# Performance work log

Hardware: AMD Instinct MI355X
Metric: run time of the kernel (lower is better)

## Reference

```python
import jax, jax.numpy as jnp
import numpy as np

DIM, R, HEAD = 512, 4, 8
HD = DIM // HEAD
SCALE = HD ** -0.5
EPS = 1e-5


def dwconv(x, w, b, stride, padding):
    # depthwise conv (groups == channels) + bias + relu; x:[B,C,H,W], w:[C,1,kh,kw]
    y = jax.lax.conv_general_dilated(
        x, w, window_strides=stride, padding=padding,
        feature_group_count=x.shape[1],
        dimension_numbers=('NCHW', 'OIHW', 'NCHW'))
    return jax.nn.relu(y + b[None, :, None, None])


def setup_inputs() -> dict:
    key = jax.random.key(0)
    ks = jax.random.split(key, 12)
    s = 0.02
    return {
        'x': jax.random.normal(ks[0], (8, DIM, 56, 56), dtype=jnp.float32),
        'Wq': jax.random.normal(ks[1], (DIM, DIM), dtype=jnp.float32) * s,
        'bq': jnp.zeros((DIM,), jnp.float32),
        'Wkv': jax.random.normal(ks[2], (2 * DIM, DIM), dtype=jnp.float32) * s,
        'bkv': jnp.zeros((2 * DIM,), jnp.float32),
        'w1a': jax.random.normal(ks[3], (DIM, 1, 1, R), dtype=jnp.float32) * s,
        'b1a': jnp.zeros((DIM,), jnp.float32),
        'w1b': jax.random.normal(ks[4], (DIM, 1, R, 1), dtype=jnp.float32) * s,
        'b1b': jnp.zeros((DIM,), jnp.float32),
        'w2': jax.random.normal(ks[5], (DIM, 1, R, R), dtype=jnp.float32) * s,
        'b2': jnp.zeros((DIM,), jnp.float32),
        'w3': jax.random.normal(ks[6], (DIM, 1, 3, 3), dtype=jnp.float32) * s,
        'b3': jnp.zeros((DIM,), jnp.float32),
        'gamma': jnp.ones((DIM,), jnp.float32),
        'beta': jnp.zeros((DIM,), jnp.float32),
    }


def reference(x, Wq, bq, Wkv, bkv, w1a, b1a, w1b, b1b, w2, b2, w3, b3, gamma, beta):
    B, C, H, W = x.shape
    N = H * W
    x_layer = x.reshape(B, C, N).transpose(0, 2, 1)  # [B,N,C]
    q = (x_layer @ Wq.T + bq).reshape(B, N, HEAD, HD).transpose(0, 2, 1, 3)  # [B,h,N,d]

    # branch 1: (1,R)s(1,R) dwconv -> (R,1)s(R,1) dwconv
    l1 = dwconv(dwconv(x, w1a, b1a, (1, R), ((0, 0), (0, 0))),
                w1b, b1b, (R, 1), ((0, 0), (0, 0))).reshape(B, C, -1)
    # branch 2: RxR stride-R dwconv
    l2 = dwconv(x, w2, b2, (R, R), ((0, 0), (0, 0))).reshape(B, C, -1)
    # branch 3: avg-pool to (H/R, W/R) then 3x3 dwconv pad 1
    l3 = x.reshape(B, C, H // R, R, W // R, R).mean(axis=(3, 5))
    l3 = dwconv(l3, w3, b3, (1, 1), ((1, 1), (1, 1))).reshape(B, C, -1)

    l_ = jnp.concatenate([l1, l2, l3], axis=2).transpose(0, 2, 1)  # [B,M,C]
    mu = l_.mean(-1, keepdims=True)
    var = ((l_ - mu) ** 2).mean(-1, keepdims=True)
    l_ = (l_ - mu) * jax.lax.rsqrt(var + EPS) * gamma + beta

    M = l_.shape[1]
    kv = (l_ @ Wkv.T + bkv).reshape(B, M, 2, HEAD, HD).transpose(2, 0, 3, 1, 4)
    k, v = kv[0], kv[1]  # [B,h,M,d]

    attn = jax.nn.softmax(jnp.einsum('bhid,bhjd->bhij', q, k) * SCALE, axis=-1)
    out = jnp.einsum('bhij,bhjd->bhid', attn, v).transpose(0, 2, 1, 3).reshape(B, N, C)
    # NOTE: original torch code computes proj(out) but then overwrites it with
    # proj_drop(out); with drop=0 the returned value is exactly `out`.
    return out
```

## Files before the change

kernel.cpp:

```cpp
#include <hip/hip_runtime.h>
#include <hip/hip_bf16.h>

#define BATCH   8
#define C_DIM   512
#define HWD     56
#define NPIX    3136
#define PW      14
#define PP      196
#define M_TOT   588
#define BM_ROWS 4704
#define BM_PAD  4736
#define HEADS   8
#define HD      64
#define N_SEQ   3136
#define SM_SCALE 0.125f
#define SM_SCALE_LOG2E 0.1803368801111204f

#define KS_STRIDE 68
#define KS_ROWS   592
#define VS_STRIDE 596
#define ATTN_LDS_SHORTS (KS_ROWS * KS_STRIDE + 64 * VS_STRIDE)
#define ATTN_LDS_BYTES  (ATTN_LDS_SHORTS * 2)

typedef __attribute__((ext_vector_type(8))) short bf16x8;
typedef __attribute__((ext_vector_type(4))) short bf16x4;
typedef __attribute__((ext_vector_type(4))) float f32x4;

__device__ __forceinline__ short f2bs(float f) {
    __hip_bfloat16 h = __float2bfloat16(f);
    return *reinterpret_cast<short*>(&h);
}
__device__ __forceinline__ unsigned pkbf(float lo, float hi) {
    __hip_bfloat162 t = __float22bfloat162_rn(make_float2(lo, hi));
    return *reinterpret_cast<unsigned*>(&t);
}
__device__ __forceinline__ float fexp2(float x) {
#if __has_builtin(__builtin_amdgcn_exp2f)
    return __builtin_amdgcn_exp2f(x);
#else
    return exp2f(x);
#endif
}

__device__ __forceinline__ f32x4 mfma16(bf16x4 a, bf16x4 b, f32x4 c) {
#if __has_builtin(__builtin_amdgcn_mfma_f32_16x16x16bf16_1k)
    return __builtin_amdgcn_mfma_f32_16x16x16bf16_1k(a, b, c, 0, 0, 0);
#elif __has_builtin(__builtin_amdgcn_mfma_f32_16x16x16_bf16)
    return __builtin_amdgcn_mfma_f32_16x16x16_bf16(a, b, c, 0, 0, 0);
#else
    asm volatile("v_mfma_f32_16x16x16_bf16 %0, %1, %2, %0\n\ts_nop 7\n\ts_nop 1"
                 : "+v"(c) : "v"(a), "v"(b));
    return c;
#endif
}

__device__ __forceinline__ void gl_lds16(const void* g, void* l) {
    __builtin_amdgcn_global_load_lds(
        (const __attribute__((address_space(1))) void*)g,
        (__attribute__((address_space(3))) void*)l, 16, 0, 0);
}


__device__ __forceinline__ void branches_body(
    int c, int b, int tid, float* sbuf,
    const float* __restrict__ x,
    const float* __restrict__ w1a, const float* __restrict__ b1a,
    const float* __restrict__ w1b, const float* __restrict__ b1b,
    const float* __restrict__ w2,  const float* __restrict__ b2,
    const float* __restrict__ w3,  const float* __restrict__ b3,
    float* __restrict__ l_pre)
{
    float* xs    = sbuf;
    float* y1s   = sbuf + 3136;
    float* pools = sbuf + 3920;
    const float* xp = x + ((size_t)(b * C_DIM + c)) * NPIX;
    for (int i = tid; i < NPIX / 4; i += 256)
        ((float4*)xs)[i] = ((const float4*)xp)[i];
    __syncthreads();

    const float wa0 = w1a[c*4+0], wa1 = w1a[c*4+1], wa2 = w1a[c*4+2], wa3 = w1a[c*4+3];
    const float ba = b1a[c];
    for (int i = tid; i < HWD * PW; i += 256) {
        int h = i / PW, w = i % PW;
        const float* r = xs + h * HWD + w * 4;
        float v = ba + r[0]*wa0 + r[1]*wa1 + r[2]*wa2 + r[3]*wa3;
        y1s[i] = fmaxf(v, 0.f);
    }
    if (tid < PP) {
        int h = tid / PW, w = tid % PW;
        float s = 0.f;
        #pragma unroll
        for (int r = 0; r < 4; ++r) {
            const float* rr = xs + (h*4 + r) * HWD + w * 4;
            s += rr[0] + rr[1] + rr[2] + rr[3];
        }
        pools[tid] = s * (1.f / 16.f);
    }
    __syncthreads();

    if (tid < PP) {
        int h = tid / PW, w = tid % PW;
        float* lp = l_pre + ((size_t)(b * C_DIM + c)) * M_TOT;
        float v1 = b1b[c];
        v1 += y1s[(h*4+0)*PW + w] * w1b[c*4+0];
        v1 += y1s[(h*4+1)*PW + w] * w1b[c*4+1];
        v1 += y1s[(h*4+2)*PW + w] * w1b[c*4+2];
        v1 += y1s[(h*4+3)*PW + w] * w1b[c*4+3];
        lp[tid] = fmaxf(v1, 0.f);
        float v2 = b2[c];
        #pragma unroll
        for (int r = 0; r < 4; ++r)
            #pragma unroll
            for (int s2 = 0; s2 < 4; ++s2)
                v2 += xs[(h*4+r)*HWD + w*4 + s2] * w2[c*16 + r*4 + s2];
        lp[PP + tid] = fmaxf(v2, 0.f);
        float v3 = b3[c];
        #pragma unroll
        for (int dh = -1; dh <= 1; ++dh)
            #pragma unroll
            for (int dw = -1; dw <= 1; ++dw) {
                int hh = h + dh, ww = w + dw;
                if (hh >= 0 && hh < PW && ww >= 0 && ww < PW)
                    v3 += pools[hh*PW + ww] * w3[c*9 + (dh+1)*3 + (dw+1)];
            }
        lp[2*PP + tid] = fmaxf(v3, 0.f);
    }
}

__device__ __forceinline__ void xpose_body(
    int bx, int by, int bz, int tid, float* sbuf,
    const float* __restrict__ x, short* __restrict__ Xb)
{
    float (*sx)[68] = (float(*)[68])sbuf;
    const int n0 = bx * 64, c0 = by * 64, b = bz;
    #pragma unroll
    for (int it = 0; it < 4; ++it) {
        int idx = tid + it * 256;
        int cr = idx >> 4, n4 = (idx & 15) * 4;
        float4 v = *(const float4*)(x + ((size_t)(b * C_DIM + c0 + cr)) * NPIX + n0 + n4);
        *(float4*)&sx[cr][n4] = v;
    }
    __syncthreads();
    #pragma unroll
    for (int p = 0; p < 2; ++p) {
        int idx = tid + p * 256;
        int nr = idx >> 3, cg = (idx & 7) * 8;
        short ov[8];
        #pragma unroll
        for (int e = 0; e < 8; ++e) ov[e] = f2bs(sx[cg + e][nr]);
        *(float4*)&Xb[((size_t)(b * NPIX + n0 + nr)) * C_DIM + c0 + cg] = *(float4*)ov;
    }
}

__device__ __forceinline__ void wconv_body(
    int blk, int tid,
    const float* __restrict__ Wq, const float* __restrict__ Wkv,
    short* __restrict__ Wqb, short* __restrict__ Wkvb)
{
    int i = (blk * 256 + tid) * 4;
    if (i < 262144) {
        float4 v = *(const float4*)(Wq + i);
        short o[4] = {f2bs(v.x), f2bs(v.y), f2bs(v.z), f2bs(v.w)};
        *(short4*)(Wqb + i) = *(short4*)o;
    } else {
        int j = i - 262144;
        float4 v = *(const float4*)(Wkv + j);
        short o[4] = {f2bs(v.x), f2bs(v.y), f2bs(v.z), f2bs(v.w)};
        *(short4*)(Wkvb + j) = *(short4*)o;
    }
}

__global__ __launch_bounds__(256) void k_front(
    const float* __restrict__ x,
    const float* __restrict__ Wq, const float* __restrict__ Wkv,
    short* __restrict__ Wqb, short* __restrict__ Wkvb,
    short* __restrict__ Xb,
    const float* __restrict__ w1a, const float* __restrict__ b1a,
    const float* __restrict__ w1b, const float* __restrict__ b1b,
    const float* __restrict__ w2,  const float* __restrict__ b2,
    const float* __restrict__ w3,  const float* __restrict__ b3,
    float* __restrict__ l_pre)
{
    __shared__ float sbuf[4368];
    const int bid = blockIdx.x, tid = threadIdx.x;
    if (bid < 4096) {
        branches_body(bid & 511, bid >> 9, tid, sbuf,
                      x, w1a, b1a, w1b, b1b, w2, b2, w3, b3, l_pre);
    } else if (bid < 7232) {
        int i2 = bid - 4096;
        xpose_body(i2 % 49, (i2 / 49) & 7, i2 / 392, tid, sbuf, x, Xb);
    } else {
        wconv_body(bid - 7232, tid, Wq, Wkv, Wqb, Wkvb);
    }
}


__device__ __forceinline__ void gemm_q_body(
    int bx, int by, int tid, short* As, short* Bs,
    const short* __restrict__ A, const short* __restrict__ Bw,
    const float* __restrict__ bias, short* __restrict__ Qb)
{
    const int lane = tid & 63, w = tid >> 6;
    const int l15 = lane & 15, quad = lane >> 4;
    const int wr = w & 1, wc = w >> 1;
    const int row0 = bx * 128, col0 = by * 128;
    const int lr8 = lane >> 3, lc8 = (lane & 7) * 8;

    f32x4 acc[4][4] = {};

    for (int c0 = 0; c0 < 512; c0 += 64) {
        __syncthreads();
        #pragma unroll
        for (int it = 0; it < 4; ++it) {
            int r = w * 32 + it * 8;
            gl_lds16(A  + (size_t)(row0 + r + lr8) * 512 + c0 + lc8, &As[r * 64]);
            gl_lds16(Bw + (size_t)(col0 + r + lr8) * 512 + c0 + lc8, &Bs[r * 64]);
        }
        __syncthreads();
        #pragma unroll
        for (int ks = 0; ks < 2; ++ks) {
            bf16x8 af[4], bf[4];
            #pragma unroll
            for (int t = 0; t < 4; ++t) {
                af[t] = *(const bf16x8*)&As[(wr*64 + t*16 + l15)*64 + ks*32 + quad*8];
                bf[t] = *(const bf16x8*)&Bs[(wc*64 + t*16 + l15)*64 + ks*32 + quad*8];
            }
            #pragma unroll
            for (int nt = 0; nt < 4; ++nt)
                #pragma unroll
                for (int mt = 0; mt < 4; ++mt)
                    acc[nt][mt] = __builtin_amdgcn_mfma_f32_16x16x32_bf16(
                        af[nt], bf[mt], acc[nt][mt], 0, 0, 0);
        }
    }

    #pragma unroll
    for (int nt = 0; nt < 4; ++nt) {
        int row_t = row0 + wr * 64 + nt * 16 + quad * 4;
        #pragma unroll
        for (int mt = 0; mt < 4; ++mt) {
            int col = col0 + wc * 64 + mt * 16 + l15;
            float bv = bias[col];
            int h = col >> 6, d = col & 63;
            #pragma unroll
            for (int r = 0; r < 4; ++r) {
                int row_g = row_t + r;
                int b = row_g / N_SEQ;
                int n = row_g - b * N_SEQ;
                Qb[(((size_t)(b * HEADS + h)) * N_SEQ + n) * HD + d] =
                    f2bs((acc[nt][mt][r] + bv) * SM_SCALE_LOG2E);
            }
        }
    }
}

__device__ __forceinline__ void stats_body(
    int sx_, int sb_, int tid, float* red,
    const float* __restrict__ l_pre, float2* __restrict__ stats)
{
    float* ssum = red;
    float* ssq  = red + 256;
    const int ml = tid & 63, cg = tid >> 6;
    const int b = sb_;
    const int m = sx_ * 64 + ml;
    float s = 0.f, q = 0.f;
    if (m < M_TOT) {
        const float* base = l_pre + ((size_t)b * C_DIM + cg * 128) * M_TOT + m;
        for (int c = 0; c < 128; ++c) {
            float v = base[(size_t)c * M_TOT];
            s += v; q += v * v;
        }
    }
    ssum[cg*64 + ml] = s; ssq[cg*64 + ml] = q;
    __syncthreads();
    if (tid < 64 && sx_ * 64 + tid < M_TOT) {
        float ts = ssum[tid] + ssum[64+tid] + ssum[128+tid] + ssum[192+tid];
        float tq = ssq[tid] + ssq[64+tid] + ssq[128+tid] + ssq[192+tid];
        float mu = ts * (1.f / 512.f);
        float var = tq * (1.f / 512.f) - mu * mu;
        stats[(size_t)b * M_TOT + sx_ * 64 + tid] =
            make_float2(mu, rsqrtf(var + 1e-5f));
    }
}

__global__ __launch_bounds__(256) void k_mid(
    const short* __restrict__ Xb, const short* __restrict__ Wqb,
    const float* __restrict__ bq, short* __restrict__ Qb,
    const float* __restrict__ l_pre, float2* __restrict__ stats)
{
    __shared__ short sb2[16384];
    const int bid = blockIdx.x, tid = threadIdx.x;
    if (bid < 784) {
        gemm_q_body(bid % 196, bid / 196, tid, sb2, sb2 + 8192,
                    Xb, Wqb, bq, Qb);
    } else {
        int sid = bid - 784;
        stats_body(sid % 10, sid / 10, tid, (float*)sb2, l_pre, stats);
    }
}

__global__ __launch_bounds__(256) void k_lnt(
    const float* __restrict__ l_pre, const float2* __restrict__ stats,
    const float* __restrict__ gamma, const float* __restrict__ beta,
    short* __restrict__ Lb)
{
    __shared__ float sx[64][68];
    const int tid = threadIdx.x;
    const int m0 = blockIdx.x * 64, c0 = blockIdx.y * 64, b = blockIdx.z;
    #pragma unroll
    for (int it = 0; it < 4; ++it) {
        int idx = tid + it * 256;
        int cr = idx >> 4, m4 = (idx & 15) * 4;
        float4 v = {0.f, 0.f, 0.f, 0.f};
        if (m0 + m4 < M_TOT)
            v = *(const float4*)(l_pre + ((size_t)(b * C_DIM + c0 + cr)) * M_TOT + m0 + m4);
        *(float4*)&sx[cr][m4] = v;
    }
    __syncthreads();
    #pragma unroll
    for (int p = 0; p < 2; ++p) {
        int idx = tid + p * 256;
        int mr = idx >> 3, cg = (idx & 7) * 8;
        int m = m0 + mr;
        float mu = 0.f, rstd = 0.f;
        if (m < M_TOT) {
            float2 st = stats[(size_t)b * M_TOT + m];
            mu = st.x; rstd = st.y;
        }
        short ov[8];
        #pragma unroll
        for (int e = 0; e < 8; ++e) {
            int c = c0 + cg + e;
            ov[e] = f2bs((sx[cg + e][mr] - mu) * rstd * gamma[c] + beta[c]);
        }
        if (m < M_TOT)
            *(float4*)&Lb[((size_t)(b * M_TOT + m)) * C_DIM + c0 + cg] = *(float4*)ov;
    }
}

__global__ __launch_bounds__(256) void k_gemm_kv(
    const short* __restrict__ A, const short* __restrict__ Bw,
    const float* __restrict__ bias,
    short* __restrict__ Kb, short* __restrict__ Vt)
{
    __shared__ short As[128 * 64];
    __shared__ short Bs[128 * 64];
    const int tid = threadIdx.x;
    const int lane = tid & 63, w = tid >> 6;
    const int l15 = lane & 15, quad = lane >> 4;
    const int wr = w & 1, wc = w >> 1;
    const int row0 = blockIdx.x * 128, col0 = blockIdx.y * 128;
    const int lr8 = lane >> 3, lc8 = (lane & 7) * 8;

    f32x4 acc[4][4] = {};

    for (int c0 = 0; c0 < 512; c0 += 64) {
        __syncthreads();
        #pragma unroll
        for (int it = 0; it < 4; ++it) {
            int r = w * 32 + it * 8;
            gl_lds16(A  + (size_t)(row0 + r + lr8) * 512 + c0 + lc8, &As[r * 64]);
            gl_lds16(Bw + (size_t)(col0 + r + lr8) * 512 + c0 + lc8, &Bs[r * 64]);
        }
        __syncthreads();
        #pragma unroll
        for (int ks = 0; ks < 2; ++ks) {
            bf16x8 af[4], bf[4];
            #pragma unroll
            for (int t = 0; t < 4; ++t) {
                af[t] = *(const bf16x8*)&As[(wr*64 + t*16 + l15)*64 + ks*32 + quad*8];
                bf[t] = *(const bf16x8*)&Bs[(wc*64 + t*16 + l15)*64 + ks*32 + quad*8];
            }
            #pragma unroll
            for (int nt = 0; nt < 4; ++nt)
                #pragma unroll
                for (int mt = 0; mt < 4; ++mt)
                    acc[nt][mt] = __builtin_amdgcn_mfma_f32_16x16x32_bf16(
                        af[nt], bf[mt], acc[nt][mt], 0, 0, 0);
        }
    }

    #pragma unroll
    for (int nt = 0; nt < 4; ++nt) {
        int row_t = row0 + wr * 64 + nt * 16 + quad * 4;
        #pragma unroll
        for (int mt = 0; mt < 4; ++mt) {
            int col = col0 + wc * 64 + mt * 16 + l15;
            float bv = bias[col];
            #pragma unroll
            for (int r = 0; r < 4; ++r) {
                int row_g = row_t + r;
                float v = acc[nt][mt][r] + bv;
                if (row_g < BM_ROWS) {
                    int b = row_g / M_TOT;
                    int m = row_g - b * M_TOT;
                    if (col < 512) {
                        int h = col >> 6, d = col & 63;
                        Kb[(((size_t)(b * HEADS + h)) * M_TOT + m) * HD + d] = f2bs(v);
                    } else {
                        int jj = col - 512, h = jj >> 6, d = jj & 63;
                        Vt[(((size_t)(b * HEADS + h)) * HD + d) * M_TOT + m] = f2bs(v);
                    }
                }
            }
        }
    }
}

__global__ __launch_bounds__(1024) void k_attn(
    const short* __restrict__ Qb, const short* __restrict__ Kb,
    const short* __restrict__ Vt, float* __restrict__ out)
{
    extern __shared__ short smem[];
    short* Ks = smem;
    short* Vs = smem + KS_ROWS * KS_STRIDE;

    const int tid = threadIdx.x;
    const int lane = tid & 63, w = tid >> 6;
    const int l15 = lane & 15, quad = lane >> 4;
    const int q4 = blockIdx.x, h = blockIdx.y, b = blockIdx.z;
    const size_t bh = (size_t)(b * HEADS + h);
    const size_t kbase = bh * M_TOT * HD;
    const size_t vbase = bh * (size_t)HD * M_TOT;

    for (int i = tid; i < 4704; i += 1024) {
        int row = i >> 3, seg = i & 7;
        *(float4*)&Ks[row * KS_STRIDE + seg * 8] =
            *(const float4*)(Kb + kbase + (size_t)row * 64 + seg * 8);
    }
    if (tid < 256) {
        int r = tid >> 6, cc = tid & 63;
        Ks[(588 + r) * KS_STRIDE + cc] = 0;
    }
    {
        int row = tid >> 4, tg = tid & 15;
        const short* src = Vt + vbase + (size_t)row * M_TOT;
        #pragma unroll 2
        for (int jj = tg; jj < 147; jj += 16)
            *(float2*)&Vs[row * VS_STRIDE + jj * 4] = *(const float2*)(src + jj * 4);
    }
    if (tid < 512) {
        int row = tid >> 3, cc = tid & 7;
        Vs[row * VS_STRIDE + 588 + cc] = 0;
    }
    __syncthreads();

    const bf16x4 ones = {(short)0x3F80, (short)0x3F80, (short)0x3F80, (short)0x3F80};

    for (int ds = w; ds < 25; ds += 16) {
        const bool sbv = (ds < 24);
        const int nA = q4 * 784 + ds * 32 + l15;
        const int nB = sbv ? nA + 16 : nA;

        bf16x8 qfA[2], qfB[2];
        #pragma unroll
        for (int ks = 0; ks < 2; ++ks) {
            qfA[ks] = *(const bf16x8*)(Qb + (bh * N_SEQ + nA) * HD + ks * 32 + quad * 8);
            qfB[ks] = *(const bf16x8*)(Qb + (bh * N_SEQ + nB) * HD + ks * 32 + quad * 8);
        }

        f32x4 oaccA[4] = {}, oaccB[4] = {};
        f32x4 rsaccA = {}, rsaccB = {};

        auto LOAD = [&](int j0, bf16x8& K0, bf16x8& K1,
                        bf16x4& V0, bf16x4& V1, bf16x4& V2, bf16x4& V3) {
            const short* kr = &Ks[(j0 + l15) * KS_STRIDE + quad * 8];
            K0 = *(const bf16x8*)kr;
            K1 = *(const bf16x8*)(kr + 32);
            const short* vr = &Vs[l15 * VS_STRIDE + j0 + quad * 4];
            V0 = *(const bf16x4*)vr;
            V1 = *(const bf16x4*)(vr + 16 * VS_STRIDE);
            V2 = *(const bf16x4*)(vr + 32 * VS_STRIDE);
            V3 = *(const bf16x4*)(vr + 48 * VS_STRIDE);
        };

        auto STEP = [&](bf16x8 K0, bf16x8 K1,
                        bf16x4 V0, bf16x4 V1, bf16x4 V2, bf16x4 V3) {
            f32x4 sA = {}, sB = {};
            __builtin_amdgcn_s_setprio(1);
            sA = __builtin_amdgcn_mfma_f32_16x16x32_bf16(K0, qfA[0], sA, 0, 0, 0);
            sB = __builtin_amdgcn_mfma_f32_16x16x32_bf16(K0, qfB[0], sB, 0, 0, 0);
            sA = __builtin_amdgcn_mfma_f32_16x16x32_bf16(K1, qfA[1], sA, 0, 0, 0);
            sB = __builtin_amdgcn_mfma_f32_16x16x32_bf16(K1, qfB[1], sB, 0, 0, 0);
            __builtin_amdgcn_s_setprio(0);

            float pA[4], pB[4];
            #pragma unroll
            for (int r = 0; r < 4; ++r) {
                pA[r] = fexp2(sA[r]);
                pB[r] = fexp2(sB[r]);
            }
            unsigned ua[2] = {pkbf(pA[0], pA[1]), pkbf(pA[2], pA[3])};
            unsigned ub[2] = {pkbf(pB[0], pB[1]), pkbf(pB[2], pB[3])};
            bf16x4 pbA, pbB;
            __builtin_memcpy(&pbA, ua, 8);
            __builtin_memcpy(&pbB, ub, 8);

            __builtin_amdgcn_s_setprio(1);
            rsaccA = mfma16(ones, pbA, rsaccA);
            rsaccB = mfma16(ones, pbB, rsaccB);

            oaccA[0] = mfma16(V0, pbA, oaccA[0]);
            oaccB[0] = mfma16(V0, pbB, oaccB[0]);
            oaccA[1] = mfma16(V1, pbA, oaccA[1]);
            oaccB[1] = mfma16(V1, pbB, oaccB[1]);
            oaccA[2] = mfma16(V2, pbA, oaccA[2]);
            oaccB[2] = mfma16(V2, pbB, oaccB[2]);
            oaccA[3] = mfma16(V3, pbA, oaccA[3]);
            oaccB[3] = mfma16(V3, pbB, oaccB[3]);
            __builtin_amdgcn_s_setprio(0);
        };

        bf16x8 k0a, k1a, k0b, k1b;
        bf16x4 v0a, v1a, v2a, v3a, v0b, v1b, v2b, v3b;

        LOAD(0, k0a, k1a, v0a, v1a, v2a, v3a);
        __builtin_amdgcn_sched_barrier(0);
        #pragma unroll 1
        for (int t = 0; t < 18; ++t) {
            const int j0 = t * 32;
            LOAD(j0 + 16, k0b, k1b, v0b, v1b, v2b, v3b);
            __builtin_amdgcn_sched_barrier(0);
            STEP(k0a, k1a, v0a, v1a, v2a, v3a);
            LOAD(j0 + 32, k0a, k1a, v0a, v1a, v2a, v3a);
            __builtin_amdgcn_sched_barrier(0);
            STEP(k0b, k1b, v0b, v1b, v2b, v3b);
        }
        STEP(k0a, k1a, v0a, v1a, v2a, v3a);

        const float invA = 1.f / (rsaccA[0] - 4.f);
        const float invB = 1.f / (rsaccB[0] - 4.f);
        float* orowA = out + ((size_t)b * N_SEQ + nA) * C_DIM + h * HD;
        #pragma unroll
        for (int dt = 0; dt < 4; ++dt) {
            float4 o;
            o.x = oaccA[dt][0] * invA; o.y = oaccA[dt][1] * invA;
            o.z = oaccA[dt][2] * invA; o.w = oaccA[dt][3] * invA;
            *(float4*)&orowA[dt * 16 + quad * 4] = o;
        }
        if (sbv) {
            float* orowB = out + ((size_t)b * N_SEQ + nB) * C_DIM + h * HD;
            #pragma unroll
            for (int dt = 0; dt < 4; ++dt) {
                float4 o;
                o.x = oaccB[dt][0] * invB; o.y = oaccB[dt][1] * invB;
                o.z = oaccB[dt][2] * invB; o.w = oaccB[dt][3] * invB;
                *(float4*)&orowB[dt * 16 + quad * 4] = o;
            }
        }
    }
}

extern "C" void kernel_launch(void* const* d_in, const int* in_sizes, int n_in,
                              void* d_out, int out_size, void* d_ws, size_t ws_size,
                              hipStream_t stream) {
    const float* x     = (const float*)d_in[0];
    const float* Wq    = (const float*)d_in[1];
    const float* bq    = (const float*)d_in[2];
    const float* Wkv   = (const float*)d_in[3];
    const float* bkv   = (const float*)d_in[4];
    const float* w1a   = (const float*)d_in[5];
    const float* b1a   = (const float*)d_in[6];
    const float* w1b   = (const float*)d_in[7];
    const float* b1b   = (const float*)d_in[8];
    const float* w2    = (const float*)d_in[9];
    const float* b2    = (const float*)d_in[10];
    const float* w3    = (const float*)d_in[11];
    const float* b3    = (const float*)d_in[12];
    const float* gamma = (const float*)d_in[13];
    const float* beta  = (const float*)d_in[14];
    float* out = (float*)d_out;

    char* ws = (char*)d_ws;
    short*  Xb    = (short*)ws;
    short*  Wqb   = (short*)(ws + 25690112);
    short*  Wkvb  = (short*)(ws + 26214400);
    float*  l_pre = (float*)(ws + 27262976);
    short*  Kb    = (short*)(ws + 27262976);
    short*  Vt    = (short*)(ws + 32079872);
    short*  Qb    = (short*)(ws + 36896768);
    float2* stats = (float2*)d_out;
    short*  Lb    = (short*)((char*)d_out + 65536);

    hipFuncSetAttribute((const void*)k_attn,
                        hipFuncAttributeMaxDynamicSharedMemorySize,
                        ATTN_LDS_BYTES);

    k_front<<<8000, 256, 0, stream>>>(
        x, Wq, Wkv, Wqb, Wkvb, Xb,
        w1a, b1a, w1b, b1b, w2, b2, w3, b3, l_pre);
    k_mid<<<864, 256, 0, stream>>>(Xb, Wqb, bq, Qb, l_pre, stats);
    k_lnt<<<dim3(10, 8, BATCH), 256, 0, stream>>>(l_pre, stats, gamma, beta, Lb);
    k_gemm_kv<<<dim3(37, 8), 256, 0, stream>>>(Lb, Wkvb, bkv, Kb, Vt);
    k_attn<<<dim3(4, HEADS, BATCH), 1024, ATTN_LDS_BYTES, stream>>>(Qb, Kb, Vt, out);
}
```

Before: 257.3 us.

## Load GEMM operands directly from global, swizzle block order, drop attention setprio

The Q and KV GEMMs stop staging tiles through LDS with global_load_lds and barriers. Each lane now reads its MFMA fragments straight from global memory, relying on L1/L2 for reuse. Block indices are remapped into groups of 8 row tiles that share column tiles, to improve L2 locality, with padding blocks that exit early. The s_setprio hints around the MFMA groups in the attention kernel are removed. The risks are more global traffic, uncoalesced 16-byte loads per lane, and a changed wave scheduling balance in attention.

After: 311.6 us. 21.1% more time.

```diff
diff --git a/kernel.cpp b/kernel.cpp
--- a/kernel.cpp
+++ b/kernel.cpp
@@ -54,12 +54,6 @@
 #endif
 }
 
-__device__ __forceinline__ void gl_lds16(const void* g, void* l) {
-    __builtin_amdgcn_global_load_lds(
-        (const __attribute__((address_space(1))) void*)g,
-        (__attribute__((address_space(3))) void*)l, 16, 0, 0);
-}
-
 
 __device__ __forceinline__ void branches_body(
     int c, int b, int tid, float* sbuf,
@@ -196,7 +190,7 @@
 
 
 __device__ __forceinline__ void gemm_q_body(
-    int bx, int by, int tid, short* As, short* Bs,
+    int bx, int by, int tid,
     const short* __restrict__ A, const short* __restrict__ Bw,
     const float* __restrict__ bias, short* __restrict__ Qb)
 {
@@ -204,34 +198,30 @@
     const int l15 = lane & 15, quad = lane >> 4;
     const int wr = w & 1, wc = w >> 1;
     const int row0 = bx * 128, col0 = by * 128;
-    const int lr8 = lane >> 3, lc8 = (lane & 7) * 8;
+
+    const short* arow[4];
+    const short* brow[4];
+    #pragma unroll
+    for (int t = 0; t < 4; ++t) {
+        arow[t] = A  + (size_t)(row0 + wr*64 + t*16 + l15) * 512 + quad * 8;
+        brow[t] = Bw + (size_t)(col0 + wc*64 + t*16 + l15) * 512 + quad * 8;
+    }
 
     f32x4 acc[4][4] = {};
-
-    for (int c0 = 0; c0 < 512; c0 += 64) {
-        __syncthreads();
-        #pragma unroll
-        for (int it = 0; it < 4; ++it) {
-            int r = w * 32 + it * 8;
-            gl_lds16(A  + (size_t)(row0 + r + lr8) * 512 + c0 + lc8, &As[r * 64]);
-            gl_lds16(Bw + (size_t)(col0 + r + lr8) * 512 + c0 + lc8, &Bs[r * 64]);
-        }
-        __syncthreads();
-        #pragma unroll
-        for (int ks = 0; ks < 2; ++ks) {
-            bf16x8 af[4], bf[4];
-            #pragma unroll
-            for (int t = 0; t < 4; ++t) {
-                af[t] = *(const bf16x8*)&As[(wr*64 + t*16 + l15)*64 + ks*32 + quad*8];
-                bf[t] = *(const bf16x8*)&Bs[(wc*64 + t*16 + l15)*64 + ks*32 + quad*8];
-            }
-            #pragma unroll
-            for (int nt = 0; nt < 4; ++nt)
-                #pragma unroll
-                for (int mt = 0; mt < 4; ++mt)
-                    acc[nt][mt] = __builtin_amdgcn_mfma_f32_16x16x32_bf16(
-                        af[nt], bf[mt], acc[nt][mt], 0, 0, 0);
-        }
+    #pragma unroll 4
+    for (int kk = 0; kk < 16; ++kk) {
+        bf16x8 af[4], bf[4];
+        #pragma unroll
+        for (int t = 0; t < 4; ++t) {
+            af[t] = *(const bf16x8*)(arow[t] + kk * 32);
+            bf[t] = *(const bf16x8*)(brow[t] + kk * 32);
+        }
+        #pragma unroll
+        for (int nt = 0; nt < 4; ++nt)
+            #pragma unroll
+            for (int mt = 0; mt < 4; ++mt)
+                acc[nt][mt] = __builtin_amdgcn_mfma_f32_16x16x32_bf16(
+                    af[nt], bf[mt], acc[nt][mt], 0, 0, 0);
     }
 
     #pragma unroll
@@ -288,14 +278,16 @@
     const float* __restrict__ bq, short* __restrict__ Qb,
     const float* __restrict__ l_pre, float2* __restrict__ stats)
 {
-    __shared__ short sb2[16384];
+    __shared__ float sred[512];
     const int bid = blockIdx.x, tid = threadIdx.x;
-    if (bid < 784) {
-        gemm_q_body(bid % 196, bid / 196, tid, sb2, sb2 + 8192,
-                    Xb, Wqb, bq, Qb);
+    if (bid < 800) {
+        int bx = (bid >> 5) * 8 + (bid & 7);
+        int by = (bid >> 3) & 3;
+        if (bx < 196)
+            gemm_q_body(bx, by, tid, Xb, Wqb, bq, Qb);
     } else {
-        int sid = bid - 784;
-        stats_body(sid % 10, sid / 10, tid, (float*)sb2, l_pre, stats);
+        int sid = bid - 800;
+        stats_body(sid % 10, sid / 10, tid, sred, l_pre, stats);
     }
 }
 
@@ -343,41 +335,39 @@
     const float* __restrict__ bias,
     short* __restrict__ Kb, short* __restrict__ Vt)
 {
-    __shared__ short As[128 * 64];
-    __shared__ short Bs[128 * 64];
-    const int tid = threadIdx.x;
+    const int bid = blockIdx.x, tid = threadIdx.x;
+    const int bx = (bid >> 6) * 8 + (bid & 7);
+    const int by = (bid >> 3) & 7;
+    if (bx >= 37) return;
+
     const int lane = tid & 63, w = tid >> 6;
     const int l15 = lane & 15, quad = lane >> 4;
     const int wr = w & 1, wc = w >> 1;
-    const int row0 = blockIdx.x * 128, col0 = blockIdx.y * 128;
-    const int lr8 = lane >> 3, lc8 = (lane & 7) * 8;
+    const int row0 = bx * 128, col0 = by * 128;
+
+    const short* arow[4];
+    const short* brow[4];
+    #pragma unroll
+    for (int t = 0; t < 4; ++t) {
+        arow[t] = A  + (size_t)(row0 + wr*64 + t*16 + l15) * 512 + quad * 8;
+        brow[t] = Bw + (size_t)(col0 + wc*64 + t*16 + l15) * 512 + quad * 8;
+    }
 
     f32x4 acc[4][4] = {};
-
-    for (int c0 = 0; c0 < 512; c0 += 64) {
-        __syncthreads();
-        #pragma unroll
-        for (int it = 0; it < 4; ++it) {
-            int r = w * 32 + it * 8;
-            gl_lds16(A  + (size_t)(row0 + r + lr8) * 512 + c0 + lc8, &As[r * 64]);
-            gl_lds16(Bw + (size_t)(col0 + r + lr8) * 512 + c0 + lc8, &Bs[r * 64]);
-        }
-        __syncthreads();
-        #pragma unroll
-        for (int ks = 0; ks < 2; ++ks) {
-            bf16x8 af[4], bf[4];
-            #pragma unroll
-            for (int t = 0; t < 4; ++t) {
-                af[t] = *(const bf16x8*)&As[(wr*64 + t*16 + l15)*64 + ks*32 + quad*8];
-                bf[t] = *(const bf16x8*)&Bs[(wc*64 + t*16 + l15)*64 + ks*32 + quad*8];
-            }
-            #pragma unroll
-            for (int nt = 0; nt < 4; ++nt)
-                #pragma unroll
-                for (int mt = 0; mt < 4; ++mt)
-                    acc[nt][mt] = __builtin_amdgcn_mfma_f32_16x16x32_bf16(
-                        af[nt], bf[mt], acc[nt][mt], 0, 0, 0);
-        }
+    #pragma unroll 4
+    for (int kk = 0; kk < 16; ++kk) {
+        bf16x8 af[4], bf[4];
+        #pragma unroll
+        for (int t = 0; t < 4; ++t) {
+            af[t] = *(const bf16x8*)(arow[t] + kk * 32);
+            bf[t] = *(const bf16x8*)(brow[t] + kk * 32);
+        }
+        #pragma unroll
+        for (int nt = 0; nt < 4; ++nt)
+            #pragma unroll
+            for (int mt = 0; mt < 4; ++mt)
+                acc[nt][mt] = __builtin_amdgcn_mfma_f32_16x16x32_bf16(
+                    af[nt], bf[mt], acc[nt][mt], 0, 0, 0);
     }
 
     #pragma unroll
@@ -477,12 +467,10 @@
         auto STEP = [&](bf16x8 K0, bf16x8 K1,
                         bf16x4 V0, bf16x4 V1, bf16x4 V2, bf16x4 V3) {
             f32x4 sA = {}, sB = {};
-            __builtin_amdgcn_s_setprio(1);
             sA = __builtin_amdgcn_mfma_f32_16x16x32_bf16(K0, qfA[0], sA, 0, 0, 0);
             sB = __builtin_amdgcn_mfma_f32_16x16x32_bf16(K0, qfB[0], sB, 0, 0, 0);
             sA = __builtin_amdgcn_mfma_f32_16x16x32_bf16(K1, qfA[1], sA, 0, 0, 0);
             sB = __builtin_amdgcn_mfma_f32_16x16x32_bf16(K1, qfB[1], sB, 0, 0, 0);
-            __builtin_amdgcn_s_setprio(0);
 
             float pA[4], pB[4];
             #pragma unroll
@@ -496,7 +484,6 @@
             __builtin_memcpy(&pbA, ua, 8);
             __builtin_memcpy(&pbB, ub, 8);
 
-            __builtin_amdgcn_s_setprio(1);
             rsaccA = mfma16(ones, pbA, rsaccA);
             rsaccB = mfma16(ones, pbB, rsaccB);
 
@@ -508,7 +495,6 @@
             oaccB[2] = mfma16(V2, pbB, oaccB[2]);
             oaccA[3] = mfma16(V3, pbA, oaccA[3]);
             oaccB[3] = mfma16(V3, pbB, oaccB[3]);
-            __builtin_amdgcn_s_setprio(0);
         };
 
         bf16x8 k0a, k1a, k0b, k1b;
@@ -589,8 +575,8 @@
     k_front<<<8000, 256, 0, stream>>>(
         x, Wq, Wkv, Wqb, Wkvb, Xb,
         w1a, b1a, w1b, b1b, w2, b2, w3, b3, l_pre);
-    k_mid<<<864, 256, 0, stream>>>(Xb, Wqb, bq, Qb, l_pre, stats);
+    k_mid<<<880, 256, 0, stream>>>(Xb, Wqb, bq, Qb, l_pre, stats);
     k_lnt<<<dim3(10, 8, BATCH), 256, 0, stream>>>(l_pre, stats, gamma, beta, Lb);
-    k_gemm_kv<<<dim3(37, 8), 256, 0, stream>>>(Lb, Wkvb, bkv, Kb, Vt);
+    k_gemm_kv<<<320, 256, 0, stream>>>(Lb, Wkvb, bkv, Kb, Vt);
     k_attn<<<dim3(4, HEADS, BATCH), 1024, ATTN_LDS_BYTES, stream>>>(Qb, Kb, Vt, out);
 }
```

## Fuse x transpose/bf16 cast into Q GEMM and LayerNorm into KV GEMM

Applied to the files above, without the earlier changes.

Removes the separate transpose pass that wrote a bf16 copy of x, and instead loads fp32 x directly in the Q GEMM A-tile loader, converting and transposing into padded LDS. LayerNorm apply plus transpose is likewise folded into the KV GEMM loader, eliminating the k_lnt kernel and the Lb intermediate. Also drops s_setprio hints in the attention inner loop. This saves one launch and a round trip of activations through global memory, at the cost of fp32 loads (twice the bytes) and reconversion per column tile in the GEMMs.

New measurement: 277.9 us. 1.08x slower.

```diff
diff --git a/kernel.cpp b/kernel.cpp
--- a/kernel.cpp
+++ b/kernel.cpp
@@ -22,6 +22,8 @@
 #define ATTN_LDS_SHORTS (KS_ROWS * KS_STRIDE + 64 * VS_STRIDE)
 #define ATTN_LDS_BYTES  (ATTN_LDS_SHORTS * 2)
 
+#define AS_STRIDE 68
+
 typedef __attribute__((ext_vector_type(8))) short bf16x8;
 typedef __attribute__((ext_vector_type(4))) short bf16x4;
 typedef __attribute__((ext_vector_type(4))) float f32x4;
@@ -127,31 +129,6 @@
     }
 }
 
-__device__ __forceinline__ void xpose_body(
-    int bx, int by, int bz, int tid, float* sbuf,
-    const float* __restrict__ x, short* __restrict__ Xb)
-{
-    float (*sx)[68] = (float(*)[68])sbuf;
-    const int n0 = bx * 64, c0 = by * 64, b = bz;
-    #pragma unroll
-    for (int it = 0; it < 4; ++it) {
-        int idx = tid + it * 256;
-        int cr = idx >> 4, n4 = (idx & 15) * 4;
-        float4 v = *(const float4*)(x + ((size_t)(b * C_DIM + c0 + cr)) * NPIX + n0 + n4);
-        *(float4*)&sx[cr][n4] = v;
-    }
-    __syncthreads();
-    #pragma unroll
-    for (int p = 0; p < 2; ++p) {
-        int idx = tid + p * 256;
-        int nr = idx >> 3, cg = (idx & 7) * 8;
-        short ov[8];
-        #pragma unroll
-        for (int e = 0; e < 8; ++e) ov[e] = f2bs(sx[cg + e][nr]);
-        *(float4*)&Xb[((size_t)(b * NPIX + n0 + nr)) * C_DIM + c0 + cg] = *(float4*)ov;
-    }
-}
-
 __device__ __forceinline__ void wconv_body(
     int blk, int tid,
     const float* __restrict__ Wq, const float* __restrict__ Wkv,
@@ -174,30 +151,26 @@
     const float* __restrict__ x,
     const float* __restrict__ Wq, const float* __restrict__ Wkv,
     short* __restrict__ Wqb, short* __restrict__ Wkvb,
-    short* __restrict__ Xb,
     const float* __restrict__ w1a, const float* __restrict__ b1a,
     const float* __restrict__ w1b, const float* __restrict__ b1b,
     const float* __restrict__ w2,  const float* __restrict__ b2,
     const float* __restrict__ w3,  const float* __restrict__ b3,
     float* __restrict__ l_pre)
 {
-    __shared__ float sbuf[4368];
+    __shared__ float sbuf[4116];
     const int bid = blockIdx.x, tid = threadIdx.x;
     if (bid < 4096) {
         branches_body(bid & 511, bid >> 9, tid, sbuf,
                       x, w1a, b1a, w1b, b1b, w2, b2, w3, b3, l_pre);
-    } else if (bid < 7232) {
-        int i2 = bid - 4096;
-        xpose_body(i2 % 49, (i2 / 49) & 7, i2 / 392, tid, sbuf, x, Xb);
     } else {
-        wconv_body(bid - 7232, tid, Wq, Wkv, Wqb, Wkvb);
+        wconv_body(bid - 4096, tid, Wq, Wkv, Wqb, Wkvb);
     }
 }
 
 
 __device__ __forceinline__ void gemm_q_body(
     int bx, int by, int tid, short* As, short* Bs,
-    const short* __restrict__ A, const short* __restrict__ Bw,
+    const float* __restrict__ x, const short* __restrict__ Bw,
     const float* __restrict__ bias, short* __restrict__ Qb)
 {
     const int lane = tid & 63, w = tid >> 6;
@@ -213,8 +186,28 @@
         #pragma unroll
         for (int it = 0; it < 4; ++it) {
             int r = w * 32 + it * 8;
-            gl_lds16(A  + (size_t)(row0 + r + lr8) * 512 + c0 + lc8, &As[r * 64]);
             gl_lds16(Bw + (size_t)(col0 + r + lr8) * 512 + c0 + lc8, &Bs[r * 64]);
+        }
+        #pragma unroll
+        for (int it = 0; it < 2; ++it) {
+            int idx = tid + it * 256;
+            int cg = (idx >> 5) * 4;
+            int n4 = (idx & 31) * 4;
+            int rg = row0 + n4;
+            int b = rg / N_SEQ, n = rg - b * N_SEQ;
+            const float* xp = x + ((size_t)(b * C_DIM) + c0 + cg) * NPIX + n;
+            float4 v0 = *(const float4*)xp;
+            float4 v1 = *(const float4*)(xp + NPIX);
+            float4 v2 = *(const float4*)(xp + 2 * NPIX);
+            float4 v3 = *(const float4*)(xp + 3 * NPIX);
+            short t0[4] = {f2bs(v0.x), f2bs(v1.x), f2bs(v2.x), f2bs(v3.x)};
+            short t1[4] = {f2bs(v0.y), f2bs(v1.y), f2bs(v2.y), f2bs(v3.y)};
+            short t2[4] = {f2bs(v0.z), f2bs(v1.z), f2bs(v2.z), f2bs(v3.z)};
+            short t3[4] = {f2bs(v0.w), f2bs(v1.w), f2bs(v2.w), f2bs(v3.w)};
+            *(short4*)&As[(n4 + 0) * AS_STRIDE + cg] = *(short4*)t0;
+            *(short4*)&As[(n4 + 1) * AS_STRIDE + cg] = *(short4*)t1;
+            *(short4*)&As[(n4 + 2) * AS_STRIDE + cg] = *(short4*)t2;
+            *(short4*)&As[(n4 + 3) * AS_STRIDE + cg] = *(short4*)t3;
         }
         __syncthreads();
         #pragma unroll
@@ -222,7 +215,7 @@
             bf16x8 af[4], bf[4];
             #pragma unroll
             for (int t = 0; t < 4; ++t) {
-                af[t] = *(const bf16x8*)&As[(wr*64 + t*16 + l15)*64 + ks*32 + quad*8];
+                af[t] = *(const bf16x8*)&As[(wr*64 + t*16 + l15)*AS_STRIDE + ks*32 + quad*8];
                 bf[t] = *(const bf16x8*)&Bs[(wc*64 + t*16 + l15)*64 + ks*32 + quad*8];
             }
             #pragma unroll
@@ -284,66 +277,28 @@
 }
 
 __global__ __launch_bounds__(256) void k_mid(
-    const short* __restrict__ Xb, const short* __restrict__ Wqb,
+    const float* __restrict__ x, const short* __restrict__ Wqb,
     const float* __restrict__ bq, short* __restrict__ Qb,
     const float* __restrict__ l_pre, float2* __restrict__ stats)
 {
-    __shared__ short sb2[16384];
+    __shared__ short smem2[16896];
     const int bid = blockIdx.x, tid = threadIdx.x;
     if (bid < 784) {
-        gemm_q_body(bid % 196, bid / 196, tid, sb2, sb2 + 8192,
-                    Xb, Wqb, bq, Qb);
+        gemm_q_body(bid % 196, bid / 196, tid, smem2, smem2 + 8704,
+                    x, Wqb, bq, Qb);
     } else {
         int sid = bid - 784;
-        stats_body(sid % 10, sid / 10, tid, (float*)sb2, l_pre, stats);
-    }
-}
-
-__global__ __launch_bounds__(256) void k_lnt(
+        stats_body(sid % 10, sid / 10, tid, (float*)smem2, l_pre, stats);
+    }
+}
+
+__global__ __launch_bounds__(256) void k_kv(
     const float* __restrict__ l_pre, const float2* __restrict__ stats,
     const float* __restrict__ gamma, const float* __restrict__ beta,
-    short* __restrict__ Lb)
-{
-    __shared__ float sx[64][68];
-    const int tid = threadIdx.x;
-    const int m0 = blockIdx.x * 64, c0 = blockIdx.y * 64, b = blockIdx.z;
-    #pragma unroll
-    for (int it = 0; it < 4; ++it) {
-        int idx = tid + it * 256;
-        int cr = idx >> 4, m4 = (idx & 15) * 4;
-        float4 v = {0.f, 0.f, 0.f, 0.f};
-        if (m0 + m4 < M_TOT)
-            v = *(const float4*)(l_pre + ((size_t)(b * C_DIM + c0 + cr)) * M_TOT + m0 + m4);
-        *(float4*)&sx[cr][m4] = v;
-    }
-    __syncthreads();
-    #pragma unroll
-    for (int p = 0; p < 2; ++p) {
-        int idx = tid + p * 256;
-        int mr = idx >> 3, cg = (idx & 7) * 8;
-        int m = m0 + mr;
-        float mu = 0.f, rstd = 0.f;
-        if (m < M_TOT) {
-            float2 st = stats[(size_t)b * M_TOT + m];
-            mu = st.x; rstd = st.y;
-        }
-        short ov[8];
-        #pragma unroll
-        for (int e = 0; e < 8; ++e) {
-            int c = c0 + cg + e;
-            ov[e] = f2bs((sx[cg + e][mr] - mu) * rstd * gamma[c] + beta[c]);
-        }
-        if (m < M_TOT)
-            *(float4*)&Lb[((size_t)(b * M_TOT + m)) * C_DIM + c0 + cg] = *(float4*)ov;
-    }
-}
-
-__global__ __launch_bounds__(256) void k_gemm_kv(
-    const short* __restrict__ A, const short* __restrict__ Bw,
-    const float* __restrict__ bias,
+    const short* __restrict__ Bw, const float* __restrict__ bias,
     short* __restrict__ Kb, short* __restrict__ Vt)
 {
-    __shared__ short As[128 * 64];
+    __shared__ short As[128 * AS_STRIDE];
     __shared__ short Bs[128 * 64];
     const int tid = threadIdx.x;
     const int lane = tid & 63, w = tid >> 6;
@@ -359,8 +314,47 @@
         #pragma unroll
         for (int it = 0; it < 4; ++it) {
             int r = w * 32 + it * 8;
-            gl_lds16(A  + (size_t)(row0 + r + lr8) * 512 + c0 + lc8, &As[r * 64]);
             gl_lds16(Bw + (size_t)(col0 + r + lr8) * 512 + c0 + lc8, &Bs[r * 64]);
+        }
+        #pragma unroll
+        for (int it = 0; it < 2; ++it) {
+            int idx = tid + it * 256;
+            int cg = (idx >> 5) * 4;
+            int m4 = (idx & 31) * 4;
+            int rg = row0 + m4;
+            short t0[4] = {}, t1[4] = {}, t2[4] = {}, t3[4] = {};
+            if (rg < BM_ROWS) {
+                int b = rg / M_TOT, m = rg - b * M_TOT;
+                const float* lp = l_pre + ((size_t)(b * C_DIM) + c0 + cg) * M_TOT + m;
+                float4 v0 = *(const float4*)lp;
+                float4 v1 = *(const float4*)(lp + M_TOT);
+                float4 v2 = *(const float4*)(lp + 2 * M_TOT);
+                float4 v3 = *(const float4*)(lp + 3 * M_TOT);
+                const float2* st = stats + (size_t)b * M_TOT + m;
+                float2 s0 = st[0], s1 = st[1], s2 = st[2], s3 = st[3];
+                float4 g4 = *(const float4*)(gamma + c0 + cg);
+                float4 b4 = *(const float4*)(beta + c0 + cg);
+                t0[0] = f2bs((v0.x - s0.x) * s0.y * g4.x + b4.x);
+                t0[1] = f2bs((v1.x - s0.x) * s0.y * g4.y + b4.y);
+                t0[2] = f2bs((v2.x - s0.x) * s0.y * g4.z + b4.z);
+                t0[3] = f2bs((v3.x - s0.x) * s0.y * g4.w + b4.w);
+                t1[0] = f2bs((v0.y - s1.x) * s1.y * g4.x + b4.x);
+                t1[1] = f2bs((v1.y - s1.x) * s1.y * g4.y + b4.y);
+                t1[2] = f2bs((v2.y - s1.x) * s1.y * g4.z + b4.z);
+                t1[3] = f2bs((v3.y - s1.x) * s1.y * g4.w + b4.w);
+                t2[0] = f2bs((v0.z - s2.x) * s2.y * g4.x + b4.x);
+                t2[1] = f2bs((v1.z - s2.x) * s2.y * g4.y + b4.y);
+                t2[2] = f2bs((v2.z - s2.x) * s2.y * g4.z + b4.z);
+                t2[3] = f2bs((v3.z - s2.x) * s2.y * g4.w + b4.w);
+                t3[0] = f2bs((v0.w - s3.x) * s3.y * g4.x + b4.x);
+                t3[1] = f2bs((v1.w - s3.x) * s3.y * g4.y + b4.y);
+                t3[2] = f2bs((v2.w - s3.x) * s3.y * g4.z + b4.z);
+                t3[3] = f2bs((v3.w - s3.x) * s3.y * g4.w + b4.w);
+            }
+            *(short4*)&As[(m4 + 0) * AS_STRIDE + cg] = *(short4*)t0;
+            *(short4*)&As[(m4 + 1) * AS_STRIDE + cg] = *(short4*)t1;
+            *(short4*)&As[(m4 + 2) * AS_STRIDE + cg] = *(short4*)t2;
+            *(short4*)&As[(m4 + 3) * AS_STRIDE + cg] = *(short4*)t3;
         }
         __syncthreads();
         #pragma unroll
@@ -368,7 +362,7 @@
             bf16x8 af[4], bf[4];
             #pragma unroll
             for (int t = 0; t < 4; ++t) {
-                af[t] = *(const bf16x8*)&As[(wr*64 + t*16 + l15)*64 + ks*32 + quad*8];
+                af[t] = *(const bf16x8*)&As[(wr*64 + t*16 + l15)*AS_STRIDE + ks*32 + quad*8];
                 bf[t] = *(const bf16x8*)&Bs[(wc*64 + t*16 + l15)*64 + ks*32 + quad*8];
             }
             #pragma unroll
@@ -477,12 +471,10 @@
         auto STEP = [&](bf16x8 K0, bf16x8 K1,
                         bf16x4 V0, bf16x4 V1, bf16x4 V2, bf16x4 V3) {
             f32x4 sA = {}, sB = {};
-            __builtin_amdgcn_s_setprio(1);
             sA = __builtin_amdgcn_mfma_f32_16x16x32_bf16(K0, qfA[0], sA, 0, 0, 0);
             sB = __builtin_amdgcn_mfma_f32_16x16x32_bf16(K0, qfB[0], sB, 0, 0, 0);
             sA = __builtin_amdgcn_mfma_f32_16x16x32_bf16(K1, qfA[1], sA, 0, 0, 0);
             sB = __builtin_amdgcn_mfma_f32_16x16x32_bf16(K1, qfB[1], sB, 0, 0, 0);
-            __builtin_amdgcn_s_setprio(0);
 
             float pA[4], pB[4];
             #pragma unroll
@@ -496,7 +488,6 @@
             __builtin_memcpy(&pbA, ua, 8);
             __builtin_memcpy(&pbB, ub, 8);
 
-            __builtin_amdgcn_s_setprio(1);
             rsaccA = mfma16(ones, pbA, rsaccA);
             rsaccB = mfma16(ones, pbB, rsaccB);
 
@@ -508,7 +499,6 @@
             oaccB[2] = mfma16(V2, pbB, oaccB[2]);
             oaccA[3] = mfma16(V3, pbA, oaccA[3]);
             oaccB[3] = mfma16(V3, pbB, oaccB[3]);
-            __builtin_amdgcn_s_setprio(0);
         };
 
         bf16x8 k0a, k1a, k0b, k1b;
@@ -572,25 +562,23 @@
     float* out = (float*)d_out;
 
     char* ws = (char*)d_ws;
-    short*  Xb    = (short*)ws;
+    float*  l_pre = (float*)ws;
     short*  Wqb   = (short*)(ws + 25690112);
     short*  Wkvb  = (short*)(ws + 26214400);
-    float*  l_pre = (float*)(ws + 27262976);
     short*  Kb    = (short*)(ws + 27262976);
     short*  Vt    = (short*)(ws + 32079872);
     short*  Qb    = (short*)(ws + 36896768);
     float2* stats = (float2*)d_out;
-    short*  Lb    = (short*)((char*)d_out + 65536);
 
     hipFuncSetAttribute((const void*)k_attn,
                         hipFuncAttributeMaxDynamicSharedMemorySize,
                         ATTN_LDS_BYTES);
 
-    k_front<<<8000, 256, 0, stream>>>(
-        x, Wq, Wkv, Wqb, Wkvb, Xb,
+    k_front<<<4864, 256, 0, stream>>>(
+        x, Wq, Wkv, Wqb, Wkvb,
         w1a, b1a, w1b, b1b, w2, b2, w3, b3, l_pre);
-    k_mid<<<864, 256, 0, stream>>>(Xb, Wqb, bq, Qb, l_pre, stats);
-    k_lnt<<<dim3(10, 8, BATCH), 256, 0, stream>>>(l_pre, stats, gamma, beta, Lb);
-    k_gemm_kv<<<dim3(37, 8), 256, 0, stream>>>(Lb, Wkvb, bkv, Kb, Vt);
+    k_mid<<<864, 256, 0, stream>>>(x, Wqb, bq, Qb, l_pre, stats);
+    k_kv<<<dim3(37, 8), 256, 0, stream>>>(
+        l_pre, stats, gamma, beta, Wkvb, bkv, Kb, Vt);
     k_attn<<<dim3(4, HEADS, BATCH), 1024, ATTN_LDS_BYTES, stream>>>(Qb, Kb, Vt, out);
 }
```

## Split attention grid finer, read V from global, drop V LDS staging

Applied to the files above, without the earlier changes.

Doubles the attention grid to 8 query chunks of 392 rows per batch-head. Each block keeps only K in LDS, so per-block shared memory shrinks and more blocks can be resident. V fragments are now loaded directly from global memory on every step, and the tail block is masked by zeroing probabilities rather than by subtracting padded exp terms. The software-pipelined LDS prefetch and the setprio hints are removed, and waves 13-15 exit right after the K load. This trades more global V traffic and less latency hiding for higher occupancy and better load balance across CUs.

After: 387.6 us. +50.6%, slower.

```diff
diff --git a/kernel.cpp b/kernel.cpp
--- a/kernel.cpp
+++ b/kernel.cpp
@@ -18,9 +18,9 @@
 
 #define KS_STRIDE 68
 #define KS_ROWS   592
-#define VS_STRIDE 596
-#define ATTN_LDS_SHORTS (KS_ROWS * KS_STRIDE + 64 * VS_STRIDE)
+#define ATTN_LDS_SHORTS (KS_ROWS * KS_STRIDE)
 #define ATTN_LDS_BYTES  (ATTN_LDS_SHORTS * 2)
+#define QROWS_PER_BLK 392
 
 typedef __attribute__((ext_vector_type(8))) short bf16x8;
 typedef __attribute__((ext_vector_type(4))) short bf16x4;
@@ -407,18 +407,17 @@
     }
 }
 
-__global__ __launch_bounds__(1024) void k_attn(
+__global__ __launch_bounds__(1024, 8) void k_attn(
     const short* __restrict__ Qb, const short* __restrict__ Kb,
     const short* __restrict__ Vt, float* __restrict__ out)
 {
     extern __shared__ short smem[];
     short* Ks = smem;
-    short* Vs = smem + KS_ROWS * KS_STRIDE;
 
     const int tid = threadIdx.x;
     const int lane = tid & 63, w = tid >> 6;
     const int l15 = lane & 15, quad = lane >> 4;
-    const int q4 = blockIdx.x, h = blockIdx.y, b = blockIdx.z;
+    const int q8 = blockIdx.x, h = blockIdx.y, b = blockIdx.z;
     const size_t bh = (size_t)(b * HEADS + h);
     const size_t kbase = bh * M_TOT * HD;
     const size_t vbase = bh * (size_t)HD * M_TOT;
@@ -432,104 +431,85 @@
         int r = tid >> 6, cc = tid & 63;
         Ks[(588 + r) * KS_STRIDE + cc] = 0;
     }
-    {
-        int row = tid >> 4, tg = tid & 15;
-        const short* src = Vt + vbase + (size_t)row * M_TOT;
-        #pragma unroll 2
-        for (int jj = tg; jj < 147; jj += 16)
-            *(float2*)&Vs[row * VS_STRIDE + jj * 4] = *(const float2*)(src + jj * 4);
-    }
-    if (tid < 512) {
-        int row = tid >> 3, cc = tid & 7;
-        Vs[row * VS_STRIDE + 588 + cc] = 0;
-    }
     __syncthreads();
 
+    if (w >= 13) return;
+
     const bf16x4 ones = {(short)0x3F80, (short)0x3F80, (short)0x3F80, (short)0x3F80};
-
-    for (int ds = w; ds < 25; ds += 16) {
-        const bool sbv = (ds < 24);
-        const int nA = q4 * 784 + ds * 32 + l15;
-        const int nB = sbv ? nA + 16 : nA;
-
-        bf16x8 qfA[2], qfB[2];
-        #pragma unroll
-        for (int ks = 0; ks < 2; ++ks) {
-            qfA[ks] = *(const bf16x8*)(Qb + (bh * N_SEQ + nA) * HD + ks * 32 + quad * 8);
-            qfB[ks] = *(const bf16x8*)(Qb + (bh * N_SEQ + nB) * HD + ks * 32 + quad * 8);
-        }
-
-        f32x4 oaccA[4] = {}, oaccB[4] = {};
-        f32x4 rsaccA = {}, rsaccB = {};
-
-        auto LOAD = [&](int j0, bf16x8& K0, bf16x8& K1,
-                        bf16x4& V0, bf16x4& V1, bf16x4& V2, bf16x4& V3) {
-            const short* kr = &Ks[(j0 + l15) * KS_STRIDE + quad * 8];
-            K0 = *(const bf16x8*)kr;
-            K1 = *(const bf16x8*)(kr + 32);
-            const short* vr = &Vs[l15 * VS_STRIDE + j0 + quad * 4];
-            V0 = *(const bf16x4*)vr;
-            V1 = *(const bf16x4*)(vr + 16 * VS_STRIDE);
-            V2 = *(const bf16x4*)(vr + 32 * VS_STRIDE);
-            V3 = *(const bf16x4*)(vr + 48 * VS_STRIDE);
-        };
-
-        auto STEP = [&](bf16x8 K0, bf16x8 K1,
-                        bf16x4 V0, bf16x4 V1, bf16x4 V2, bf16x4 V3) {
-            f32x4 sA = {}, sB = {};
-            __builtin_amdgcn_s_setprio(1);
-            sA = __builtin_amdgcn_mfma_f32_16x16x32_bf16(K0, qfA[0], sA, 0, 0, 0);
-            sB = __builtin_amdgcn_mfma_f32_16x16x32_bf16(K0, qfB[0], sB, 0, 0, 0);
-            sA = __builtin_amdgcn_mfma_f32_16x16x32_bf16(K1, qfA[1], sA, 0, 0, 0);
-            sB = __builtin_amdgcn_mfma_f32_16x16x32_bf16(K1, qfB[1], sB, 0, 0, 0);
-            __builtin_amdgcn_s_setprio(0);
-
-            float pA[4], pB[4];
-            #pragma unroll
-            for (int r = 0; r < 4; ++r) {
-                pA[r] = fexp2(sA[r]);
-                pB[r] = fexp2(sB[r]);
-            }
-            unsigned ua[2] = {pkbf(pA[0], pA[1]), pkbf(pA[2], pA[3])};
-            unsigned ub[2] = {pkbf(pB[0], pB[1]), pkbf(pB[2], pB[3])};
-            bf16x4 pbA, pbB;
-            __builtin_memcpy(&pbA, ua, 8);
-            __builtin_memcpy(&pbB, ub, 8);
-
-            __builtin_amdgcn_s_setprio(1);
-            rsaccA = mfma16(ones, pbA, rsaccA);
-            rsaccB = mfma16(ones, pbB, rsaccB);
-
-            oaccA[0] = mfma16(V0, pbA, oaccA[0]);
-            oaccB[0] = mfma16(V0, pbB, oaccB[0]);
-            oaccA[1] = mfma16(V1, pbA, oaccA[1]);
-            oaccB[1] = mfma16(V1, pbB, oaccB[1]);
-            oaccA[2] = mfma16(V2, pbA, oaccA[2]);
-            oaccB[2] = mfma16(V2, pbB, oaccB[2]);
-            oaccA[3] = mfma16(V3, pbA, oaccA[3]);
-            oaccB[3] = mfma16(V3, pbB, oaccB[3]);
-            __builtin_amdgcn_s_setprio(0);
-        };
-
-        bf16x8 k0a, k1a, k0b, k1b;
-        bf16x4 v0a, v1a, v2a, v3a, v0b, v1b, v2b, v3b;
-
-        LOAD(0, k0a, k1a, v0a, v1a, v2a, v3a);
-        __builtin_amdgcn_sched_barrier(0);
-        #pragma unroll 1
-        for (int t = 0; t < 18; ++t) {
-            const int j0 = t * 32;
-            LOAD(j0 + 16, k0b, k1b, v0b, v1b, v2b, v3b);
-            __builtin_amdgcn_sched_barrier(0);
-            STEP(k0a, k1a, v0a, v1a, v2a, v3a);
-            LOAD(j0 + 32, k0a, k1a, v0a, v1a, v2a, v3a);
-            __builtin_amdgcn_sched_barrier(0);
-            STEP(k0b, k1b, v0b, v1b, v2b, v3b);
-        }
-        STEP(k0a, k1a, v0a, v1a, v2a, v3a);
-
-        const float invA = 1.f / (rsaccA[0] - 4.f);
-        const float invB = 1.f / (rsaccB[0] - 4.f);
+    const float tmask = (quad == 3) ? 0.f : 1.f;
+
+    const int rA = w * 32 + l15;
+    const int rB = rA + 16;
+    int nA = q8 * QROWS_PER_BLK + rA; if (nA > N_SEQ - 1) nA = N_SEQ - 1;
+    int nB = q8 * QROWS_PER_BLK + rB; if (nB > N_SEQ - 1) nB = N_SEQ - 1;
+    const bool stA = (rA < QROWS_PER_BLK);
+    const bool stB = (rB < QROWS_PER_BLK);
+
+    bf16x8 qfA[2], qfB[2];
+    #pragma unroll
+    for (int ks = 0; ks < 2; ++ks) {
+        qfA[ks] = *(const bf16x8*)(Qb + (bh * N_SEQ + nA) * HD + ks * 32 + quad * 8);
+        qfB[ks] = *(const bf16x8*)(Qb + (bh * N_SEQ + nB) * HD + ks * 32 + quad * 8);
+    }
+
+    f32x4 oaccA[4] = {}, oaccB[4] = {};
+    f32x4 rsaccA = {}, rsaccB = {};
+
+    const short* vp0 = Vt + vbase + (size_t)l15 * M_TOT + quad * 4;
+
+    auto STEP = [&](int j0, bool tail) {
+        const short* vp = vp0 + j0;
+        bf16x4 v0 = *(const bf16x4*)(vp);
+        bf16x4 v1 = *(const bf16x4*)(vp + 16 * M_TOT);
+        bf16x4 v2 = *(const bf16x4*)(vp + 32 * M_TOT);
+        bf16x4 v3 = *(const bf16x4*)(vp + 48 * M_TOT);
+
+        const short* kr = &Ks[(j0 + l15) * KS_STRIDE + quad * 8];
+        bf16x8 kf0 = *(const bf16x8*)kr;
+        bf16x8 kf1 = *(const bf16x8*)(kr + 32);
+
+        f32x4 sA = {}, sB = {};
+        sA = __builtin_amdgcn_mfma_f32_16x16x32_bf16(kf0, qfA[0], sA, 0, 0, 0);
+        sB = __builtin_amdgcn_mfma_f32_16x16x32_bf16(kf0, qfB[0], sB, 0, 0, 0);
+        sA = __builtin_amdgcn_mfma_f32_16x16x32_bf16(kf1, qfA[1], sA, 0, 0, 0);
+        sB = __builtin_amdgcn_mfma_f32_16x16x32_bf16(kf1, qfB[1], sB, 0, 0, 0);
+
+        float pA[4], pB[4];
+        #pragma unroll
+        for (int r = 0; r < 4; ++r) {
+            pA[r] = fexp2(sA[r]);
+            pB[r] = fexp2(sB[r]);
+        }
+        if (tail) {
+            #pragma unroll
+            for (int r = 0; r < 4; ++r) { pA[r] *= tmask; pB[r] *= tmask; }
+        }
+        unsigned ua[2] = {pkbf(pA[0], pA[1]), pkbf(pA[2], pA[3])};
+        unsigned ub[2] = {pkbf(pB[0], pB[1]), pkbf(pB[2], pB[3])};
+        bf16x4 pbA, pbB;
+        __builtin_memcpy(&pbA, ua, 8);
+        __builtin_memcpy(&pbB, ub, 8);
+
+        rsaccA = mfma16(ones, pbA, rsaccA);
+        rsaccB = mfma16(ones, pbB, rsaccB);
+
+        oaccA[0] = mfma16(v0, pbA, oaccA[0]);
+        oaccB[0] = mfma16(v0, pbB, oaccB[0]);
+        oaccA[1] = mfma16(v1, pbA, oaccA[1]);
+        oaccB[1] = mfma16(v1, pbB, oaccB[1]);
+        oaccA[2] = mfma16(v2, pbA, oaccA[2]);
+        oaccB[2] = mfma16(v2, pbB, oaccB[2]);
+        oaccA[3] = mfma16(v3, pbA, oaccA[3]);
+        oaccB[3] = mfma16(v3, pbB, oaccB[3]);
+    };
+
+    #pragma unroll 1
+    for (int j0 = 0; j0 < 576; j0 += 16) STEP(j0, false);
+    STEP(576, true);
+
+    const float invA = 1.f / rsaccA[0];
+    const float invB = 1.f / rsaccB[0];
+    if (stA) {
         float* orowA = out + ((size_t)b * N_SEQ + nA) * C_DIM + h * HD;
         #pragma unroll
         for (int dt = 0; dt < 4; ++dt) {
@@ -538,15 +518,15 @@
             o.z = oaccA[dt][2] * invA; o.w = oaccA[dt][3] * invA;
             *(float4*)&orowA[dt * 16 + quad * 4] = o;
         }
-        if (sbv) {
-            float* orowB = out + ((size_t)b * N_SEQ + nB) * C_DIM + h * HD;
-            #pragma unroll
-            for (int dt = 0; dt < 4; ++dt) {
-                float4 o;
-                o.x = oaccB[dt][0] * invB; o.y = oaccB[dt][1] * invB;
-                o.z = oaccB[dt][2] * invB; o.w = oaccB[dt][3] * invB;
-                *(float4*)&orowB[dt * 16 + quad * 4] = o;
-            }
+    }
+    if (stB) {
+        float* orowB = out + ((size_t)b * N_SEQ + nB) * C_DIM + h * HD;
+        #pragma unroll
+        for (int dt = 0; dt < 4; ++dt) {
+            float4 o;
+            o.x = oaccB[dt][0] * invB; o.y = oaccB[dt][1] * invB;
+            o.z = oaccB[dt][2] * invB; o.w = oaccB[dt][3] * invB;
+            *(float4*)&orowB[dt * 16 + quad * 4] = o;
         }
     }
 }
@@ -592,5 +572,5 @@
     k_mid<<<864, 256, 0, stream>>>(Xb, Wqb, bq, Qb, l_pre, stats);
     k_lnt<<<dim3(10, 8, BATCH), 256, 0, stream>>>(l_pre, stats, gamma, beta, Lb);
     k_gemm_kv<<<dim3(37, 8), 256, 0, stream>>>(Lb, Wkvb, bkv, Kb, Vt);
-    k_attn<<<dim3(4, HEADS, BATCH), 1024, ATTN_LDS_BYTES, stream>>>(Qb, Kb, Vt, out);
-}
+    k_attn<<<dim3(8, HEADS, BATCH), 1024, ATTN_LDS_BYTES, stream>>>(Qb, Kb, Vt, out);
+}
```
